# Kernel optimization log

Measured on AMD Instinct MI355X. Metric: run time of the kernel, lower is better.

The kernel has to match this reference:

```python
import jax, jax.numpy as jnp
from jax import lax
import numpy as np

ALPHA = 0.5
MAX_ITERS = 40
TOL = 1e-6
BITS = 8


def fake_quant_sym(w, bits=BITS):
    # symmetric per-tensor fake quantisation
    qmax = float(2 ** (bits - 1) - 1)
    scale = jnp.max(jnp.abs(w)) / qmax
    return jnp.round(w / scale) * scale


def fb_solve(Wq, Uq, bq, x, alpha=ALPHA, max_iters=MAX_ITERS, tol=TOL):
    # forward-backward splitting fixed-point solve: z = relu((1-a)z + a(Wz + Ux^T + b))
    n = Wq.shape[0]
    B = x.shape[0]
    Ux = Uq @ x.T + bq[:, None]  # (n, B), constant across iterations

    def cond(carry):
        z, res, it = carry
        return jnp.logical_and(it < max_iters, res >= tol)

    def body(carry):
        z, _, it = carry
        u = (1.0 - alpha) * z + alpha * (Wq @ z + Ux)
        z_next = jax.nn.relu(u)  # relu_prox
        res = jnp.linalg.norm(z_next - z) / (jnp.linalg.norm(z) + 1e-12)
        return z_next, res, it + 1

    z0 = jnp.zeros((n, B), dtype=x.dtype)
    z, _, _ = lax.while_loop(cond, body, (z0, jnp.array(jnp.inf, dtype=x.dtype), 0))
    u_star = (1.0 - alpha) * z + alpha * (Wq @ z + Ux)
    mask = (u_star > 0).astype(x.dtype)  # relu Jacobian mask D*
    return z, mask


def setup_inputs() -> dict:
    key = jax.random.key(0)
    k0, k1, k2, k3, k4 = jax.random.split(key, 5)
    n, d, B, C = 512, 784, 128, 10
    # scale W so ||W||_2 < 1 (monotone operator condition m > 0)
    W = 0.3 * jax.random.normal(k0, (n, n), dtype=jnp.float32) / jnp.sqrt(n)
    U = jax.random.normal(k1, (n, d), dtype=jnp.float32) / jnp.sqrt(d)
    b = 0.01 * jax.random.normal(k2, (n,), dtype=jnp.float32)
    x = jax.random.normal(k3, (B, d), dtype=jnp.float32)
    Wc = jax.random.normal(k4, (C, n), dtype=jnp.float32) / jnp.sqrt(n)
    bc = jnp.zeros((C,), dtype=jnp.float32)
    return {"W": W, "U": U, "b": b, "x": x, "Wc": Wc, "bc": bc}


def reference(W, U, b, x, Wc, bc):
    # post-training fake quantisation of W, U, b (done once at init in torch)
    Wq = fake_quant_sym(W)
    Uq = fake_quant_sym(U)
    bq = fake_quant_sym(b)
    z_star, _ = fb_solve(Wq, Uq, bq, x)  # (n, B)
    logits = z_star.T @ Wc.T + bc  # classifier on z*^T
    return logits
```

## Files before the change

### kernel.cpp

```cpp
#include <hip/hip_runtime.h>
#include <hip/hip_bf16.h>


#define N_DIM 512
#define D_DIM 784
#define B_DIM 128
#define C_DIM 10
#define QMAX 127.0f
#define N_ITERS 40
#define HILO_START 28
#define ZPITCH 528
#define MT 4
#define UPITCH 808

typedef int    i32x4  __attribute__((ext_vector_type(4)));
typedef float  f32x4  __attribute__((ext_vector_type(4)));
typedef __bf16 bf16x8 __attribute__((ext_vector_type(8)));
typedef short  s16x2  __attribute__((ext_vector_type(2)));

__device__ __forceinline__ float pscale64(const float* __restrict__ p) {
    float m = 0.0f;
#pragma unroll 16
    for (int i = 0; i < 64; ++i) m = fmaxf(m, p[i]);
    return m * (1.0f / QMAX);
}

__device__ __forceinline__ void pack_hl(const int vq[4], unsigned int& h, unsigned int& l) {
    int pk01, pk23;
#if __has_builtin(__builtin_amdgcn_cvt_pk_i16)
    union { s16x2 v; int i; } u0, u1;
    u0.v = __builtin_amdgcn_cvt_pk_i16(vq[0], vq[1]);
    u1.v = __builtin_amdgcn_cvt_pk_i16(vq[2], vq[3]);
    pk01 = u0.i; pk23 = u1.i;
#else
    asm("v_cvt_pk_i16_i32 %0, %1, %2" : "=v"(pk01) : "v"(vq[0]), "v"(vq[1]));
    asm("v_cvt_pk_i16_i32 %0, %1, %2" : "=v"(pk23) : "v"(vq[2]), "v"(vq[3]));
#endif
    h = __builtin_amdgcn_perm((unsigned int)pk23, (unsigned int)pk01, 0x07050301u);
    l = __builtin_amdgcn_perm((unsigned int)pk23, (unsigned int)pk01, 0x06040200u) ^ 0x80808080u;
}

__global__ void maxabs_kernel(const float* __restrict__ W,
                              const float* __restrict__ U,
                              const float* __restrict__ b,
                              float* __restrict__ partials) {
    const float4* src;
    int n4;
    if (blockIdx.y == 0)      { src = (const float4*)W; n4 = N_DIM * N_DIM / 4; }
    else if (blockIdx.y == 1) { src = (const float4*)U; n4 = N_DIM * D_DIM / 4; }
    else                      { src = (const float4*)b; n4 = N_DIM / 4; }
    float m = 0.0f;
    for (int i = blockIdx.x * blockDim.x + threadIdx.x; i < n4; i += gridDim.x * blockDim.x) {
        float4 v = src[i];
        m = fmaxf(m, fmaxf(fmaxf(fabsf(v.x), fabsf(v.y)), fmaxf(fabsf(v.z), fabsf(v.w))));
    }
    __shared__ float red[256];
    red[threadIdx.x] = m;
    __syncthreads();
    for (int s = 128; s > 0; s >>= 1) {
        if (threadIdx.x < s) red[threadIdx.x] = fmaxf(red[threadIdx.x], red[threadIdx.x + s]);
        __syncthreads();
    }
    if (threadIdx.x == 0) partials[blockIdx.y * 64 + blockIdx.x] = red[0];
}

__global__ __launch_bounds__(256) void prep_kernel(const float* __restrict__ W,
                                                   const float* __restrict__ U,
                                                   const float* __restrict__ b,
                                                   const float* __restrict__ x,
                                                   const float* __restrict__ partials,
                                                   signed char* __restrict__ Qp8,
                                                   float* __restrict__ UxT) {
    __shared__ __bf16 xhS[16][UPITCH];
    __shared__ __bf16 xlS[16][UPITCH];
    __shared__ f32x4  sacc[4][64];
    const int t = threadIdx.x;
    if (blockIdx.x < 256) {
        const float s = pscale64(partials);
        const float inv = 1.0f / s;
        int idx = blockIdx.x * 256 + t;
        float4 w = ((const float4*)W)[idx];
        int k = (idx << 2) & (N_DIM - 1);
        int r = (idx << 2) >> 9;
        char4 c;
        c.x = (signed char)(int)rintf(w.x * inv);
        c.y = (signed char)(int)rintf(w.y * inv);
        c.z = (signed char)(int)rintf(w.z * inv);
        c.w = (signed char)(int)rintf(w.w * inv);
        int kc = k >> 6, q = (k >> 4) & 3, jj = k & 15;
        *(char4*)&Qp8[((kc << 9) + r) * 64 + q * 16 + jj] = c;
    } else {
        const float sU = pscale64(partials + 64);
        const float invU = 1.0f / sU;
        const float sb = pscale64(partials + 128);
        const int bx = blockIdx.x - 256;
        const int i0 = (bx >> 3) * 16;
        const int c0 = (bx & 7) * 16;
        for (int i = t; i < 16 * 196; i += 256) {
            int r = i / 196, kf = i - r * 196;
            float4 v = *(const float4*)&x[(c0 + r) * D_DIM + (kf << 2)];
            union { __bf16 e[4]; ushort4 u; } hh, ll;
            float f0 = v.x, f1 = v.y, f2 = v.z, f3 = v.w;
            __bf16 h0 = (__bf16)f0, h1 = (__bf16)f1, h2 = (__bf16)f2, h3 = (__bf16)f3;
            hh.e[0] = h0; hh.e[1] = h1; hh.e[2] = h2; hh.e[3] = h3;
            ll.e[0] = (__bf16)(f0 - (float)h0);
            ll.e[1] = (__bf16)(f1 - (float)h1);
            ll.e[2] = (__bf16)(f2 - (float)h2);
            ll.e[3] = (__bf16)(f3 - (float)h3);
            *(ushort4*)&xhS[r][kf << 2] = hh.u;
            *(ushort4*)&xlS[r][kf << 2] = ll.u;
        }
        {
            int r = t >> 4, k = D_DIM + (t & 15);
            xhS[r][k] = (__bf16)0.0f; xlS[r][k] = (__bf16)0.0f;
        }
        __syncthreads();
        const int wave = t >> 6, lane = t & 63;
        const int m = lane & 15, quad = lane >> 4;
        f32x4 acc = {};
        for (int kc = wave; kc < 25; kc += 4) {
            const int k0 = (kc << 5) + (quad << 3);
            bf16x8 au = {};
            if (k0 < D_DIM) {
                const float4 u0 = *(const float4*)&U[(i0 + m) * D_DIM + k0];
                const float4 u1 = *(const float4*)&U[(i0 + m) * D_DIM + k0 + 4];
                au[0] = (__bf16)rintf(u0.x * invU); au[1] = (__bf16)rintf(u0.y * invU);
                au[2] = (__bf16)rintf(u0.z * invU); au[3] = (__bf16)rintf(u0.w * invU);
                au[4] = (__bf16)rintf(u1.x * invU); au[5] = (__bf16)rintf(u1.y * invU);
                au[6] = (__bf16)rintf(u1.z * invU); au[7] = (__bf16)rintf(u1.w * invU);
            }
            bf16x8 bh = *(const bf16x8*)&xhS[m][k0];
            bf16x8 bl = *(const bf16x8*)&xlS[m][k0];
            acc = __builtin_amdgcn_mfma_f32_16x16x32_bf16(au, bh, acc, 0, 0, 0);
            acc = __builtin_amdgcn_mfma_f32_16x16x32_bf16(au, bl, acc, 0, 0, 0);
        }
        sacc[wave][lane] = acc;
        __syncthreads();
        if (wave == 0) {
            f32x4 s0 = sacc[0][lane], s1 = sacc[1][lane];
            f32x4 s2 = sacc[2][lane], s3 = sacc[3][lane];
            const int row0 = i0 + (quad << 2);
            f32x4 o;
#pragma unroll
            for (int r = 0; r < 4; ++r)
                o[r] = sU * (s0[r] + s1[r] + s2[r] + s3[r])
                     + rintf(b[row0 + r] / sb) * sb;
            *(f32x4*)&UxT[(c0 + m) * N_DIM + row0] = o;
        }
    }
}

__global__ __launch_bounds__(512, 2) void solve_kernel(const signed char* __restrict__ Qp8,
                                                       const float* __restrict__ UxT,
                                                       const float* __restrict__ partials,
                                                       const float* __restrict__ Wc,
                                                       const float* __restrict__ bc,
                                                       float* __restrict__ out) {
    __shared__ signed char zh[2][16][ZPITCH];
    __shared__ signed char zl[2][16][ZPITCH];
    __shared__ float red[32][16][C_DIM];
    const int t = threadIdx.x;
    const int wave = t >> 6;
    const int lane = t & 63;
    const int m = lane & 15;
    const int quad = lane >> 4;
    const int c0 = blockIdx.x * 16;
    const float sW = pscale64(partials);
    const float c1 = sW * (1.0f / 2048.0f);
    const float hc_hi = c1 * 128.0f;
    const float hc_lo = c1 * 0.5f;
    const int rowbase = wave * 64;

    i32x4 A[MT][8];
#pragma unroll
    for (int ti = 0; ti < MT; ++ti)
#pragma unroll
        for (int kc = 0; kc < 8; ++kc)
            A[ti][kc] = *(const i32x4*)&Qp8[((kc << 9) + rowbase + ti * 16 + m) * 64 + (quad << 4)];

    const i32x4 onesb = {0x01010101, 0x01010101, 0x01010101, 0x01010101};
    i32x4 rs[MT];
#pragma unroll
    for (int ti = 0; ti < MT; ++ti) {
        i32x4 a = {};
#pragma unroll
        for (int kc = 0; kc < 8; ++kc)
            a = __builtin_amdgcn_mfma_i32_16x16x64_i8(A[ti][kc], onesb, a, 0, 0, 0);
        rs[ti] = a;
    }

    float zreg[MT][4];
    float uxh[MT][4];
#pragma unroll
    for (int ti = 0; ti < MT; ++ti) {
        const int row0 = rowbase + ti * 16 + (quad << 2);
        const f32x4 v4 = *(const f32x4*)&UxT[(c0 + m) * N_DIM + row0];
        int vq[4];
#pragma unroll
        for (int r = 0; r < 4; ++r) {
            const float v = v4[r];
            uxh[ti][r] = 0.5f * (v + hc_hi * (float)rs[ti][r]);
            const float z1 = fmaxf(0.5f * v, 0.0f);
            zreg[ti][r] = z1;
            vq[r] = (int)rintf(z1 * 2048.0f);
        }
        unsigned int h, l;
        pack_hl(vq, h, l);
        *(unsigned int*)&zh[0][m][row0] = h;
        *(unsigned int*)&zl[0][m][row0] = l;
    }

#pragma unroll
    for (int ti = 0; ti < MT; ++ti)
#pragma unroll
        for (int kc = 0; kc < 8; ++kc)
            asm volatile("" : "+v"(A[ti][kc]));
    __syncthreads();

    int cur = 0;
    for (int it = 1; it < N_ITERS; ++it) {
        const bool lo = (it >= HILO_START);
        const bool wlo = (it >= HILO_START - 1);
        i32x4 acch[MT] = {};
        i32x4 accl[MT] = {};
        if (lo) {
#pragma unroll
            for (int kc = 0; kc < 8; ++kc) {
                i32x4 bh = *(const i32x4*)&zh[cur][m][(kc << 6) + (quad << 4)];
                i32x4 bl = *(const i32x4*)&zl[cur][m][(kc << 6) + (quad << 4)];
#pragma unroll
                for (int ti = 0; ti < MT; ++ti) {
                    acch[ti] = __builtin_amdgcn_mfma_i32_16x16x64_i8(A[ti][kc], bh, acch[ti], 0, 0, 0);
                    accl[ti] = __builtin_amdgcn_mfma_i32_16x16x64_i8(A[ti][kc], bl, accl[ti], 0, 0, 0);
                }
            }
        } else {
#pragma unroll
            for (int kc = 0; kc < 8; ++kc) {
                i32x4 bh = *(const i32x4*)&zh[cur][m][(kc << 6) + (quad << 4)];
#pragma unroll
                for (int ti = 0; ti < MT; ++ti)
                    acch[ti] = __builtin_amdgcn_mfma_i32_16x16x64_i8(A[ti][kc], bh, acch[ti], 0, 0, 0);
            }
        }
        const int nxt = cur ^ 1;
#pragma unroll
        for (int ti = 0; ti < MT; ++ti) {
            const int row0 = rowbase + ti * 16 + (quad << 2);
            int vq[4];
#pragma unroll
            for (int r = 0; r < 4; ++r) {
                float base = fmaf(0.5f, zreg[ti][r], uxh[ti][r]);
                float u = lo ? fmaf(hc_hi, (float)acch[ti][r], fmaf(hc_lo, (float)accl[ti][r], base))
                             : fmaf(hc_hi, (float)acch[ti][r], base);
                float zn = fmaxf(u, 0.0f);
                zreg[ti][r] = zn;
                vq[r] = (int)rintf(zn * 2048.0f);
            }
            unsigned int h, l;
            pack_hl(vq, h, l);
            *(unsigned int*)&zh[nxt][m][row0] = h;
            if (wlo) *(unsigned int*)&zl[nxt][m][row0] = l;
        }
        __syncthreads();
        cur = nxt;
    }

    {
        const int grp = wave * 4 + quad;
        float p[C_DIM];
#pragma unroll
        for (int cl = 0; cl < C_DIM; ++cl) p[cl] = 0.0f;
#pragma unroll
        for (int ti = 0; ti < MT; ++ti) {
            const int row0 = rowbase + ti * 16 + (quad << 2);
#pragma unroll
            for (int r = 0; r < 4; ++r) {
                float zv = zreg[ti][r];
#pragma unroll
                for (int cl = 0; cl < C_DIM; ++cl)
                    p[cl] += zv * Wc[cl * N_DIM + row0 + r];
            }
        }
#pragma unroll
        for (int cl = 0; cl < C_DIM; ++cl) red[grp][m][cl] = p[cl];
        __syncthreads();
        for (int s = 16; s > 0; s >>= 1) {
            if (grp < s) {
#pragma unroll
                for (int cl = 0; cl < C_DIM; ++cl)
                    red[grp][m][cl] += red[grp + s][m][cl];
            }
            __syncthreads();
        }
        if (t < 16 * C_DIM) {
            int col = t & 15;
            int cl  = t >> 4;
            out[(c0 + col) * C_DIM + cl] = red[0][col][cl] + bc[cl];
        }
    }
}

extern "C" void kernel_launch(void* const* d_in, const int* in_sizes, int n_in,
                              void* d_out, int out_size, void* d_ws, size_t ws_size,
                              hipStream_t stream) {
    const float* W  = (const float*)d_in[0];
    const float* U  = (const float*)d_in[1];
    const float* b  = (const float*)d_in[2];
    const float* x  = (const float*)d_in[3];
    const float* Wc = (const float*)d_in[4];
    const float* bc = (const float*)d_in[5];
    float* out = (float*)d_out;

    float* ws = (float*)d_ws;
    float* partials = ws;
    signed char* Qp8 = (signed char*)(ws + 256);
    float* UxT = ws + 256 + (N_DIM * N_DIM / 4);

    maxabs_kernel<<<dim3(64, 3), 256, 0, stream>>>(W, U, b, partials);
    prep_kernel<<<512, 256, 0, stream>>>(W, U, b, x, partials, Qp8, UxT);
    solve_kernel<<<8, 512, 0, stream>>>(Qp8, UxT, partials, Wc, bc, out);
}
```

Before: 142.3 us.

## Fuse maxabs into prep via grid barrier; widen solve to 1024 threads

Removes the separate maxabs kernel. Each prep block now computes per-block abs-max values, combines them with global atomicMax, and waits at a spin-based grid barrier before quantising. This relies on all 512 blocks being co-resident, which deadlocks if that does not hold. The solve kernel goes from 512 to 1024 threads with half the row tiles per wave (MT 4→2), which lowers per-thread register load and gives more waves for latency hiding. It also keeps z in a pre-scaled ×2048 domain to save multiplies and replaces the epilogue LDS reduction with wave shuffles.

```diff
diff --git a/kernel.cpp b/kernel.cpp
--- a/kernel.cpp
+++ b/kernel.cpp
@@ -10,20 +10,13 @@
 #define N_ITERS 40
 #define HILO_START 28
 #define ZPITCH 528
-#define MT 4
+#define MT 2
 #define UPITCH 808
 
 typedef int    i32x4  __attribute__((ext_vector_type(4)));
 typedef float  f32x4  __attribute__((ext_vector_type(4)));
 typedef __bf16 bf16x8 __attribute__((ext_vector_type(8)));
 typedef short  s16x2  __attribute__((ext_vector_type(2)));
-
-__device__ __forceinline__ float pscale64(const float* __restrict__ p) {
-    float m = 0.0f;
-#pragma unroll 16
-    for (int i = 0; i < 64; ++i) m = fmaxf(m, p[i]);
-    return m * (1.0f / QMAX);
-}
 
 __device__ __forceinline__ void pack_hl(const int vq[4], unsigned int& h, unsigned int& l) {
     int pk01, pk23;
@@ -40,43 +33,64 @@
     l = __builtin_amdgcn_perm((unsigned int)pk23, (unsigned int)pk01, 0x06040200u) ^ 0x80808080u;
 }
 
-__global__ void maxabs_kernel(const float* __restrict__ W,
-                              const float* __restrict__ U,
-                              const float* __restrict__ b,
-                              float* __restrict__ partials) {
-    const float4* src;
-    int n4;
-    if (blockIdx.y == 0)      { src = (const float4*)W; n4 = N_DIM * N_DIM / 4; }
-    else if (blockIdx.y == 1) { src = (const float4*)U; n4 = N_DIM * D_DIM / 4; }
-    else                      { src = (const float4*)b; n4 = N_DIM / 4; }
-    float m = 0.0f;
-    for (int i = blockIdx.x * blockDim.x + threadIdx.x; i < n4; i += gridDim.x * blockDim.x) {
-        float4 v = src[i];
-        m = fmaxf(m, fmaxf(fmaxf(fabsf(v.x), fabsf(v.y)), fmaxf(fabsf(v.z), fabsf(v.w))));
-    }
-    __shared__ float red[256];
-    red[threadIdx.x] = m;
-    __syncthreads();
-    for (int s = 128; s > 0; s >>= 1) {
-        if (threadIdx.x < s) red[threadIdx.x] = fmaxf(red[threadIdx.x], red[threadIdx.x + s]);
-        __syncthreads();
-    }
-    if (threadIdx.x == 0) partials[blockIdx.y * 64 + blockIdx.x] = red[0];
-}
-
 __global__ __launch_bounds__(256) void prep_kernel(const float* __restrict__ W,
                                                    const float* __restrict__ U,
                                                    const float* __restrict__ b,
                                                    const float* __restrict__ x,
-                                                   const float* __restrict__ partials,
+                                                   int* __restrict__ sync,
                                                    signed char* __restrict__ Qp8,
                                                    float* __restrict__ UxT) {
     __shared__ __bf16 xhS[16][UPITCH];
     __shared__ __bf16 xlS[16][UPITCH];
     __shared__ f32x4  sacc[4][64];
+    __shared__ float  smax[3];
     const int t = threadIdx.x;
+    const int wave = t >> 6, lane = t & 63;
+
+    {
+        const int gid = blockIdx.x * 256 + t;
+        float mW = 0.0f, mU = 0.0f, mB = 0.0f;
+        if (gid < N_DIM * N_DIM / 4) {
+            float4 v = ((const float4*)W)[gid];
+            mW = fmaxf(fmaxf(fabsf(v.x), fabsf(v.y)), fmaxf(fabsf(v.z), fabsf(v.w)));
+        }
+        if (gid < N_DIM * D_DIM / 4) {
+            float4 v = ((const float4*)U)[gid];
+            mU = fmaxf(fmaxf(fabsf(v.x), fabsf(v.y)), fmaxf(fabsf(v.z), fabsf(v.w)));
+        }
+        if (gid < N_DIM / 4) {
+            float4 v = ((const float4*)b)[gid];
+            mB = fmaxf(fmaxf(fabsf(v.x), fabsf(v.y)), fmaxf(fabsf(v.z), fabsf(v.w)));
+        }
+#pragma unroll
+        for (int s = 1; s < 64; s <<= 1) {
+            mW = fmaxf(mW, __shfl_xor(mW, s));
+            mU = fmaxf(mU, __shfl_xor(mU, s));
+            mB = fmaxf(mB, __shfl_xor(mB, s));
+        }
+        float* ls = (float*)sacc;
+        if (lane == 0) { ls[wave * 3 + 0] = mW; ls[wave * 3 + 1] = mU; ls[wave * 3 + 2] = mB; }
+        __syncthreads();
+        if (t == 0) {
+            float aW = fmaxf(fmaxf(ls[0], ls[3]), fmaxf(ls[6], ls[9]));
+            float aU = fmaxf(fmaxf(ls[1], ls[4]), fmaxf(ls[7], ls[10]));
+            float aB = fmaxf(fmaxf(ls[2], ls[5]), fmaxf(ls[8], ls[11]));
+            atomicMax(&sync[1], __float_as_int(aW));
+            atomicMax(&sync[2], __float_as_int(aU));
+            atomicMax(&sync[3], __float_as_int(aB));
+            __hip_atomic_fetch_add(&sync[0], 1, __ATOMIC_ACQ_REL, __HIP_MEMORY_SCOPE_AGENT);
+            while (__hip_atomic_load(&sync[0], __ATOMIC_ACQUIRE, __HIP_MEMORY_SCOPE_AGENT)
+                   < (int)gridDim.x)
+                __builtin_amdgcn_s_sleep(2);
+            smax[0] = __int_as_float(__hip_atomic_load(&sync[1], __ATOMIC_RELAXED, __HIP_MEMORY_SCOPE_AGENT));
+            smax[1] = __int_as_float(__hip_atomic_load(&sync[2], __ATOMIC_RELAXED, __HIP_MEMORY_SCOPE_AGENT));
+            smax[2] = __int_as_float(__hip_atomic_load(&sync[3], __ATOMIC_RELAXED, __HIP_MEMORY_SCOPE_AGENT));
+        }
+        __syncthreads();
+    }
+
     if (blockIdx.x < 256) {
-        const float s = pscale64(partials);
+        const float s = smax[0] * (1.0f / QMAX);
         const float inv = 1.0f / s;
         int idx = blockIdx.x * 256 + t;
         float4 w = ((const float4*)W)[idx];
@@ -90,9 +104,9 @@
         int kc = k >> 6, q = (k >> 4) & 3, jj = k & 15;
         *(char4*)&Qp8[((kc << 9) + r) * 64 + q * 16 + jj] = c;
     } else {
-        const float sU = pscale64(partials + 64);
+        const float sU = smax[1] * (1.0f / QMAX);
         const float invU = 1.0f / sU;
-        const float sb = pscale64(partials + 128);
+        const float sb = smax[2] * (1.0f / QMAX);
         const int bx = blockIdx.x - 256;
         const int i0 = (bx >> 3) * 16;
         const int c0 = (bx & 7) * 16;
@@ -115,7 +129,6 @@
             xhS[r][k] = (__bf16)0.0f; xlS[r][k] = (__bf16)0.0f;
         }
         __syncthreads();
-        const int wave = t >> 6, lane = t & 63;
         const int m = lane & 15, quad = lane >> 4;
         f32x4 acc = {};
         for (int kc = wave; kc < 25; kc += 4) {
@@ -150,26 +163,27 @@
     }
 }
 
-__global__ __launch_bounds__(512, 2) void solve_kernel(const signed char* __restrict__ Qp8,
-                                                       const float* __restrict__ UxT,
-                                                       const float* __restrict__ partials,
-                                                       const float* __restrict__ Wc,
-                                                       const float* __restrict__ bc,
-                                                       float* __restrict__ out) {
+__global__ __launch_bounds__(1024, 1) void solve_kernel(const signed char* __restrict__ Qp8,
+                                                        const float* __restrict__ UxT,
+                                                        const float* __restrict__ wsf,
+                                                        const float* __restrict__ Wc,
+                                                        const float* __restrict__ bc,
+                                                        float* __restrict__ out) {
     __shared__ signed char zh[2][16][ZPITCH];
     __shared__ signed char zl[2][16][ZPITCH];
-    __shared__ float red[32][16][C_DIM];
+    __shared__ float red[16][16][C_DIM];
     const int t = threadIdx.x;
     const int wave = t >> 6;
     const int lane = t & 63;
     const int m = lane & 15;
     const int quad = lane >> 4;
     const int c0 = blockIdx.x * 16;
-    const float sW = pscale64(partials);
+    const float sW = wsf[1] * (1.0f / QMAX);
     const float c1 = sW * (1.0f / 2048.0f);
     const float hc_hi = c1 * 128.0f;
-    const float hc_lo = c1 * 0.5f;
-    const int rowbase = wave * 64;
+    const float g_hi = sW * 128.0f;
+    const float g_lo = sW * 0.5f;
+    const int rowbase = wave * 32;
 
     i32x4 A[MT][8];
 #pragma unroll
@@ -189,8 +203,8 @@
         rs[ti] = a;
     }
 
-    float zreg[MT][4];
-    float uxh[MT][4];
+    float Z[MT][4];
+    float UX2[MT][4];
 #pragma unroll
     for (int ti = 0; ti < MT; ++ti) {
         const int row0 = rowbase + ti * 16 + (quad << 2);
@@ -199,10 +213,12 @@
 #pragma unroll
         for (int r = 0; r < 4; ++r) {
             const float v = v4[r];
-            uxh[ti][r] = 0.5f * (v + hc_hi * (float)rs[ti][r]);
+            const float uxh = 0.5f * (v + hc_hi * (float)rs[ti][r]);
+            UX2[ti][r] = uxh * 2048.0f;
             const float z1 = fmaxf(0.5f * v, 0.0f);
-            zreg[ti][r] = z1;
-            vq[r] = (int)rintf(z1 * 2048.0f);
+            const float Z1 = z1 * 2048.0f;
+            Z[ti][r] = Z1;
+            vq[r] = (int)rintf(Z1);
         }
         unsigned int h, l;
         pack_hl(vq, h, l);
@@ -250,12 +266,12 @@
             int vq[4];
 #pragma unroll
             for (int r = 0; r < 4; ++r) {
-                float base = fmaf(0.5f, zreg[ti][r], uxh[ti][r]);
-                float u = lo ? fmaf(hc_hi, (float)acch[ti][r], fmaf(hc_lo, (float)accl[ti][r], base))
-                             : fmaf(hc_hi, (float)acch[ti][r], base);
-                float zn = fmaxf(u, 0.0f);
-                zreg[ti][r] = zn;
-                vq[r] = (int)rintf(zn * 2048.0f);
+                float base = fmaf(0.5f, Z[ti][r], UX2[ti][r]);
+                float u = lo ? fmaf(g_hi, (float)acch[ti][r], fmaf(g_lo, (float)accl[ti][r], base))
+                             : fmaf(g_hi, (float)acch[ti][r], base);
+                float Zn = fmaxf(u, 0.0f);
+                Z[ti][r] = Zn;
+                vq[r] = (int)rintf(Zn);
             }
             unsigned int h, l;
             pack_hl(vq, h, l);
@@ -267,7 +283,6 @@
     }
 
     {
-        const int grp = wave * 4 + quad;
         float p[C_DIM];
 #pragma unroll
         for (int cl = 0; cl < C_DIM; ++cl) p[cl] = 0.0f;
@@ -276,20 +291,27 @@
             const int row0 = rowbase + ti * 16 + (quad << 2);
 #pragma unroll
             for (int r = 0; r < 4; ++r) {
-                float zv = zreg[ti][r];
+                float zv = Z[ti][r] * (1.0f / 2048.0f);
 #pragma unroll
                 for (int cl = 0; cl < C_DIM; ++cl)
                     p[cl] += zv * Wc[cl * N_DIM + row0 + r];
             }
         }
 #pragma unroll
-        for (int cl = 0; cl < C_DIM; ++cl) red[grp][m][cl] = p[cl];
-        __syncthreads();
-        for (int s = 16; s > 0; s >>= 1) {
-            if (grp < s) {
+        for (int cl = 0; cl < C_DIM; ++cl) {
+            p[cl] += __shfl_xor(p[cl], 16);
+            p[cl] += __shfl_xor(p[cl], 32);
+        }
+        if (lane < 16) {
+#pragma unroll
+            for (int cl = 0; cl < C_DIM; ++cl) red[wave][lane][cl] = p[cl];
+        }
+        __syncthreads();
+        for (int s = 8; s > 0; s >>= 1) {
+            if (wave < s && lane < 16) {
 #pragma unroll
                 for (int cl = 0; cl < C_DIM; ++cl)
-                    red[grp][m][cl] += red[grp + s][m][cl];
+                    red[wave][lane][cl] += red[wave + s][lane][cl];
             }
             __syncthreads();
         }
@@ -313,11 +335,11 @@
     float* out = (float*)d_out;
 
     float* ws = (float*)d_ws;
-    float* partials = ws;
+    int* sync = (int*)ws;
     signed char* Qp8 = (signed char*)(ws + 256);
     float* UxT = ws + 256 + (N_DIM * N_DIM / 4);
 
-    maxabs_kernel<<<dim3(64, 3), 256, 0, stream>>>(W, U, b, partials);
-    prep_kernel<<<512, 256, 0, stream>>>(W, U, b, x, partials, Qp8, UxT);
-    solve_kernel<<<8, 512, 0, stream>>>(Qp8, UxT, partials, Wc, bc, out);
+    hipMemsetAsync(sync, 0, 16, stream);
+    prep_kernel<<<512, 256, 0, stream>>>(W, U, b, x, sync, Qp8, UxT);
+    solve_kernel<<<8, 1024, 0, stream>>>(Qp8, UxT, ws, Wc, bc, out);
 }
```

Result: slower. 161.9 us (+13.7%).
